# Kernel optimization log

Measured on AMD Instinct MI355X. Metric: run time of the kernel, lower is better.

## Reference

```python
import jax, jax.numpy as jnp
import numpy as np

B, T, D = 2, 2048, 2048
NH, NKV = 16, 4
HD = D // NH  # 128
BASE, TSL = 10000.0, 1024


def rotary_tables(T, hd, base=BASE, tsl=TSL):
    # Matches Rotary.forward with rd == hd (rd=0 in __init__ -> full head dim).
    ar = jnp.arange(0, hd, 2, dtype=jnp.float32) / hd
    if T <= tsl:
        inv = 1.0 / (base ** ar)
    else:
        # NTK-style rescale; note right-assoc exponent in original torch code:
        # 1/(base * (T/tsl) ** ((rd/(rd-2)) ** ar))
        inv = 1.0 / (base * jnp.power(T / tsl, jnp.power(hd / (hd - 2.0), ar)))
    f = jnp.outer(jnp.arange(T, dtype=jnp.float32), inv)  # [T, hd//2]
    cos = jnp.cos(f)[None, :, None, :]  # [1,T,1,hd//2]
    sin = jnp.sin(f)[None, :, None, :]
    return cos, sin


def apply_rope(x, cos, sin):
    # full-dim rope: split halves, rotate
    h = x.shape[-1] // 2
    x1, x2 = x[..., :h], x[..., h:]
    return jnp.concatenate((x1 * cos + x2 * sin, -x1 * sin + x2 * cos), axis=-1)


def rms_norm(x):
    eps = jnp.finfo(x.dtype).eps
    return x * jax.lax.rsqrt(jnp.mean(x * x, axis=-1, keepdims=True) + eps)


def setup_inputs() -> dict:
    key = jax.random.key(0)
    k0, k1, k2, k3, k4 = jax.random.split(key, 5)
    s = 0.02
    return {
        "x": jax.random.normal(k0, (B, T, D), jnp.float32),
        "qw": jax.random.normal(k1, (NH * HD, D), jnp.float32) * s,
        "kw": jax.random.normal(k2, (NKV * HD, D), jnp.float32) * s,
        "vw": jax.random.normal(k3, (NKV * HD, D), jnp.float32) * s,
        "ow": jax.random.normal(k4, (D, D), jnp.float32) * s,
        "qg": jnp.ones((NH,), jnp.float32),
    }


def reference(x, qw, kw, vw, ow, qg):
    Bx, Tx, Dx = x.shape
    q = (x @ qw.T).reshape(Bx, Tx, NH, HD)
    k = (x @ kw.T).reshape(Bx, Tx, NKV, HD)
    v = (x @ vw.T).reshape(Bx, Tx, NKV, HD)
    q = rms_norm(q)
    k = rms_norm(k)
    cos, sin = rotary_tables(Tx, HD)
    q = apply_rope(q, cos, sin) * qg[None, None, :, None]
    k = apply_rope(k, cos, sin)
    # GQA: repeat kv heads
    r = NH // NKV
    k = jnp.repeat(k, r, axis=2)  # [B,T,NH,HD]
    v = jnp.repeat(v, r, axis=2)
    scale = 1.0 / jnp.sqrt(jnp.asarray(HD, q.dtype))
    scores = jnp.einsum("bqhd,bkhd->bhqk", q, k) * scale  # [B,NH,T,T]
    causal = jnp.tril(jnp.ones((Tx, Tx), dtype=bool))
    scores = jnp.where(causal[None, None, :, :], scores, jnp.asarray(-jnp.inf, scores.dtype))
    attn = jax.nn.softmax(scores, axis=-1)
    y = jnp.einsum("bhqk,bkhd->bqhd", attn, v)  # [B,T,NH,HD]
    return y.reshape(Bx, Tx, Dx) @ ow.T
```

## Files before the change

### kernel.cpp

```cpp
#include <hip/hip_runtime.h>
#include <hip/hip_bf16.h>
#include <stdint.h>


typedef __attribute__((ext_vector_type(8))) short short8;
typedef __attribute__((ext_vector_type(4))) float f32x4;
typedef __attribute__((ext_vector_type(16))) float f32x16;

#define GLOAD16(gp, lp) \
  __builtin_amdgcn_global_load_lds((const __attribute__((address_space(1))) void*)(gp), \
                                   (__attribute__((address_space(3))) void*)(lp), 16, 0, 0)

#define BAR() do { asm volatile("" ::: "memory"); __builtin_amdgcn_s_barrier(); asm volatile("" ::: "memory"); } while (0)

__device__ __forceinline__ float bf2f(unsigned short u) {
  union { unsigned int i; float f; } v; v.i = ((unsigned int)u) << 16; return v.f;
}
__device__ __forceinline__ unsigned short f2bf(float f) {
  union { float fl; unsigned int i; } v; v.fl = f;
  unsigned int r = v.i + 0x7fffu + ((v.i >> 16) & 1u);
  return (unsigned short)(r >> 16);
}
__device__ __forceinline__ unsigned pk2(float a, float b) {
  return (unsigned)f2bf(a) | ((unsigned)f2bf(b) << 16);
}

__global__ __launch_bounds__(256) void prep_kernel(
    const float* __restrict__ x, const float* __restrict__ qw,
    const float* __restrict__ kw, const float* __restrict__ vw,
    const float* __restrict__ ow,
    unsigned short* __restrict__ xb, unsigned short* __restrict__ wqkv,
    unsigned short* __restrict__ owb, float* __restrict__ cost, float* __restrict__ sint) {
  const int NX = 2097152;
  const int NW = 1572864;
  const int NO = 1048576;
  const int NT = 131072;
  int tid = blockIdx.x * 256 + threadIdx.x;
  if (tid < NX) {
    float4 v = ((const float4*)x)[tid];
    uint2 o; o.x = pk2(v.x, v.y); o.y = pk2(v.z, v.w);
    ((uint2*)xb)[tid] = o;
  } else if (tid < NX + NW) {
    int i = tid - NX; int e = i * 4;
    const float* src = (e < 4194304) ? (qw + e)
                     : (e < 5242880) ? (kw + (e - 4194304))
                                     : (vw + (e - 5242880));
    float4 v = *(const float4*)src;
    uint2 o; o.x = pk2(v.x, v.y); o.y = pk2(v.z, v.w);
    ((uint2*)wqkv)[i] = o;
  } else if (tid < NX + NW + NO) {
    int i = tid - NX - NW;
    float4 v = ((const float4*)ow)[i];
    uint2 o; o.x = pk2(v.x, v.y); o.y = pk2(v.z, v.w);
    ((uint2*)owb)[i] = o;
  } else if (tid < NX + NW + NO + NT) {
    int i = tid - NX - NW - NO;
    int t = i >> 6, j = i & 63;
    float e = exp2f(0.02272008f * (float)j * (1.0f / 64.0f));
    float inv = 1.0f / (10000.0f * exp2f(e));
    float f = (float)t * inv;
    cost[i] = cosf(f);
    sint[i] = sinf(f);
  }
}

template <int IM, int OUTF>
__global__ __launch_bounds__(512) void gemm8ph(const unsigned short* __restrict__ A,
                                               const unsigned short* __restrict__ Bw,
                                               void* __restrict__ Cp,
                                               int MT, int NTn, int N, int K) {
  extern __shared__ char smc[];
  constexpr int S = IM * 8;
  constexpr int IQ = IM / 2;
  constexpr int ASZ = IM * 2048;
  constexpr int DB = 2 * ASZ + 32768;
  constexpr int AL = (IM * 128) / 512;
  const int tid = threadIdx.x;
  const int l = tid & 63, w = tid >> 6;
  const int lane_r = l & 15, lane_g = l >> 4;
  const int wr = w >> 2, wc = w & 3;

  int qch = (MT * NTn) >> 3;
  int orig = blockIdx.x;
  int wgid = (orig & 7) * qch + (orig >> 3);
  int by = wgid / NTn, bx = wgid - by * NTn;
  const int m0 = by * IM * 32, n0 = bx * 256;

  f32x4 acc[IM][4];
#pragma unroll
  for (int i = 0; i < IM; ++i)
#pragma unroll
    for (int j = 0; j < 4; ++j) acc[i][j] = {0.f, 0.f, 0.f, 0.f};

  const unsigned short* srcA[AL]; int ldA[AL];
#pragma unroll
  for (int t = 0; t < AL; ++t) {
    int idx = t * 512 + tid;
    int rc = idx >> 3, kc = idx & 7;
    int wrp = rc >= S ? 1 : 0, rr = rc & (S - 1);
    int row = wrp * 2 * S + rr;
    srcA[t] = A + (size_t)(m0 + row) * K + (kc ^ (rc & 7)) * 8;
    ldA[t] = idx * 16;
  }
  const unsigned short* srcB[2]; int ldB[2];
#pragma unroll
  for (int t = 0; t < 2; ++t) {
    int idx = t * 512 + tid;
    int rc = idx >> 3, kc = idx & 7;
    int nrow = (rc >> 5) * 64 + (rc & 31);
    srcB[t] = Bw + (size_t)(n0 + nrow) * K + (kc ^ (rc & 7)) * 8;
    ldB[t] = idx * 16;
  }
  const int SK = S * K, JK = 32 * K;

  auto STA = [&](int kt, int ih, int dqb) {
    char* d = smc + dqb + ih * ASZ;
#pragma unroll
    for (int t = 0; t < AL; ++t) GLOAD16(srcA[t] + kt + ih * SK, d + ldA[t]);
  };
  auto STB = [&](int kt, int jh, int dqb) {
    char* d = smc + dqb + 2 * ASZ + jh * 16384;
#pragma unroll
    for (int t = 0; t < 2; ++t) GLOAD16(srcB[t] + kt + jh * JK, d + ldB[t]);
  };

  int oA[IQ][2], oB[2][2];
#pragma unroll
  for (int iq = 0; iq < IQ; ++iq)
#pragma unroll
    for (int ks = 0; ks < 2; ++ks) {
      int rc = wr * S + iq * 16 + lane_r;
      oA[iq][ks] = rc * 128 + ((ks * 64 + lane_g * 16) ^ ((rc & 7) << 4));
    }
#pragma unroll
  for (int jj = 0; jj < 2; ++jj)
#pragma unroll
    for (int ks = 0; ks < 2; ++ks) {
      int rc = wc * 32 + jj * 16 + lane_r;
      oB[jj][ks] = rc * 128 + ((ks * 64 + lane_g * 16) ^ ((rc & 7) << 4));
    }

#define VMC() do { if constexpr (IM == 8) asm volatile("s_waitcnt vmcnt(6)" ::: "memory"); \
                   else                   asm volatile("s_waitcnt vmcnt(5)" ::: "memory"); } while (0)
#define VM0() asm volatile("s_waitcnt vmcnt(0)" ::: "memory")
#define MM(IH, JH, BR) do { \
    __builtin_amdgcn_s_setprio(1); \
    _Pragma("unroll") \
    for (int iq = 0; iq < IQ; ++iq) \
      _Pragma("unroll") \
      for (int jj = 0; jj < 2; ++jj) \
        _Pragma("unroll") \
        for (int ks = 0; ks < 2; ++ks) \
          acc[(IH) * IQ + iq][(JH) * 2 + jj] = __builtin_amdgcn_mfma_f32_16x16x32_bf16( \
              af[iq][ks], BR[jj][ks], acc[(IH) * IQ + iq][(JH) * 2 + jj], 0, 0, 0); \
    __builtin_amdgcn_s_setprio(0); } while (0)

  const int NS = K >> 6;
  STA(0, 0, 0); STB(0, 0, 0); STB(0, 1, 0); STA(0, 1, 0);
  STA(64, 0, DB); STB(64, 0, DB); STB(64, 1, DB);
  VMC();
  BAR();

#pragma unroll 1
  for (int s = 0; s < NS; ++s) {
    const int dq = (s & 1) * DB, dn = DB - dq;
    const char* Ab = smc + dq;
    const char* Bb = Ab + 2 * ASZ;
    short8 af[IQ][2], b0[2][2], b1[2][2];
    if (s + 1 < NS) STA((s + 1) << 6, 1, dn);
#pragma unroll
    for (int iq = 0; iq < IQ; ++iq)
#pragma unroll
      for (int ks = 0; ks < 2; ++ks) af[iq][ks] = *(const short8*)(Ab + oA[iq][ks]);
#pragma unroll
    for (int jj = 0; jj < 2; ++jj)
#pragma unroll
      for (int ks = 0; ks < 2; ++ks) b0[jj][ks] = *(const short8*)(Bb + oB[jj][ks]);
    MM(0, 0, b0);
    BAR();
    if (s + 2 < NS) STA((s + 2) << 6, 0, dq);
#pragma unroll
    for (int jj = 0; jj < 2; ++jj)
#pragma unroll
      for (int ks = 0; ks < 2; ++ks) b1[jj][ks] = *(const short8*)(Bb + 16384 + oB[jj][ks]);
    MM(0, 1, b1);
    BAR();
    if (s + 2 < NS) STB((s + 2) << 6, 0, dq);
#pragma unroll
    for (int iq = 0; iq < IQ; ++iq)
#pragma unroll
      for (int ks = 0; ks < 2; ++ks) af[iq][ks] = *(const short8*)(Ab + ASZ + oA[iq][ks]);
    MM(1, 0, b0);
    BAR();
    if (s + 2 < NS) STB((s + 2) << 6, 1, dq);
    MM(1, 1, b1);
    if (s + 2 < NS) VMC(); else VM0();
    BAR();
  }
#undef VMC
#undef VM0
#undef MM

#pragma unroll
  for (int ih = 0; ih < 2; ++ih)
#pragma unroll
    for (int iq = 0; iq < IQ; ++iq) {
      int row = m0 + wr * 2 * S + ih * S + iq * 16 + lane_g * 4;
#pragma unroll
      for (int j = 0; j < 4; ++j) {
        int col = n0 + wc * 64 + j * 16 + lane_r;
#pragma unroll
        for (int r = 0; r < 4; ++r) {
          float v = acc[ih * IQ + iq][j][r];
          if (OUTF)
            ((float*)Cp)[(size_t)(row + r) * N + col] = v;
          else
            ((unsigned short*)Cp)[(size_t)(row + r) * N + col] = f2bf(v);
        }
      }
    }
}

__global__ __launch_bounds__(256) void normrope_kernel(unsigned short* __restrict__ qkv,
                                                       const float* __restrict__ cost,
                                                       const float* __restrict__ sint,
                                                       const float* __restrict__ qg) {
  const int tid = threadIdx.x, l = tid & 63, w = tid >> 6;
  int row = blockIdx.x * 4 + w;
  int tok = row / 20, hh = row - tok * 20;
  int t = tok & 2047;
  bool isq = hh < 16;
  int col0 = isq ? hh * 128 : 2048 + (hh - 16) * 128;
  unsigned short* p = qkv + (size_t)tok * 3072 + col0 + 2 * l;
  unsigned int u = *(const unsigned int*)p;
  float x0 = bf2f((unsigned short)(u & 0xffffu));
  float x1 = bf2f((unsigned short)(u >> 16));
  float ss = x0 * x0 + x1 * x1;
#pragma unroll
  for (int m = 1; m < 64; m <<= 1) ss += __shfl_xor(ss, m);
  float rn = rsqrtf(ss * (1.0f / 128.0f) + 1.1920928955078125e-07f);
  float n0 = x0 * rn, n1 = x1 * rn;
  float p0 = __shfl_xor(n0, 32);
  float p1 = __shfl_xor(n1, 32);
  int jj = (2 * l) & 63;
  float c0 = cost[t * 64 + jj], c1 = cost[t * 64 + jj + 1];
  float s0 = sint[t * 64 + jj], s1 = sint[t * 64 + jj + 1];
  float o0, o1;
  if (l < 32) { o0 = n0 * c0 + p0 * s0; o1 = n1 * c1 + p1 * s1; }
  else        { o0 = -p0 * s0 + n0 * c0; o1 = -p1 * s1 + n1 * c1; }
  if (isq) { float g = qg[hh] * 0.08838834764831845f * 1.4426950408889634f; o0 *= g; o1 *= g; }
  *(unsigned int*)p = pk2(o0, o1);
}

__global__ __launch_bounds__(256) void vtrans_kernel(const unsigned short* __restrict__ qkv,
                                                     unsigned short* __restrict__ vtg) {
  __shared__ unsigned short tile[64][132];
  int bid = blockIdx.x;
  int pan = bid & 7, tt = bid >> 3;
  int b = pan >> 2, kvh = pan & 3;
  int t0 = tt * 64;
  const unsigned short* src = qkv + ((size_t)(b * 2048 + t0)) * 3072 + 2560 + kvh * 128;
#pragma unroll
  for (int i = 0; i < 8; ++i) {
    int idx = i * 256 + threadIdx.x;
    int row = idx >> 5, c4 = idx & 31;
    uint2 v = *(const uint2*)(src + (size_t)row * 3072 + c4 * 4);
    *(uint2*)&tile[row][c4 * 4] = v;
  }
  __syncthreads();
  unsigned short* dst = vtg + (size_t)pan * 262144 + t0;
#pragma unroll
  for (int i = 0; i < 8; ++i) {
    int idx = i * 256 + threadIdx.x;
    int d = idx >> 4, tc = idx & 15;
    unsigned short a0 = tile[tc * 4 + 0][d], a1 = tile[tc * 4 + 1][d];
    unsigned short a2 = tile[tc * 4 + 2][d], a3 = tile[tc * 4 + 3][d];
    uint2 o; o.x = (unsigned)a0 | ((unsigned)a1 << 16);
    o.y = (unsigned)a2 | ((unsigned)a3 << 16);
    *(uint2*)(dst + (size_t)d * 2048 + tc * 4) = o;
  }
}

__global__ __launch_bounds__(256, 2) void attn_fa5(const unsigned short* __restrict__ qkv,
                                                   const unsigned short* __restrict__ vtg,
                                                   unsigned short* __restrict__ y) {
  extern __shared__ char smc[];
  const int tid = threadIdx.x;
  const int l = tid & 63, w = tid >> 6;
  const int lq = l & 31, hi = l >> 5;

  int n = blockIdx.x;
  int pan = n & 7;
  int b = pan >> 2, kvh = pan & 3;
  int idx2 = n >> 3;
  int h = kvh * 4 + (idx2 & 3);
  int pairIdx = idx2 >> 2;
  const size_t rowbase = (size_t)b * 2048;
  const unsigned short* kvK = qkv + rowbase * 3072;
  const unsigned short* vtp = vtg + (size_t)pan * 262144;

  int kg[4], vg[4], sl[4];
#pragma unroll
  for (int t = 0; t < 4; ++t) {
    int idx = t * 256 + tid;
    { int row = idx >> 4, c = idx & 15, gc = c ^ (row & 7);
      kg[t] = row * 3072 + 2048 + kvh * 128 + gc * 8; }
    { int d = idx >> 3, c = idx & 7, gc = c ^ (d & 7);
      vg[t] = d * 2048 + gc * 8; }
    sl[t] = idx * 16;
  }
  const int swq = (lq & 7) << 4;
  int oxd[8];
#pragma unroll
  for (int ds = 0; ds < 8; ++ds) oxd[ds] = (ds * 32 + hi * 16) ^ swq;
  const int krow = lq * 256;
  const int vrow = lq * 128;
  const int pbase = 65536 + w * 4096;
  const int prow = pbase + lq * 128;
  int opw[2][4];
#pragma unroll
  for (int t = 0; t < 2; ++t)
#pragma unroll
    for (int m = 0; m < 4; ++m) opw[t][m] = prow + ((t * 64 + m * 16 + hi * 8) ^ swq);

  auto STAGE = [&](int tile, int bufsel) {
    const unsigned short* srcK = kvK + (size_t)tile * 64 * 3072;
    const unsigned short* srcV = vtp + tile * 64;
    char* kd = smc + bufsel * 16384;
    char* vd = smc + 32768 + bufsel * 16384;
#pragma unroll
    for (int t = 0; t < 4; ++t) {
      GLOAD16(srcK + kg[t], kd + sl[t]);
      GLOAD16(srcV + vg[t], vd + sl[t]);
    }
  };

#pragma unroll 1
  for (int phase = 0; phase < 2; ++phase) {
    const int qt = phase ? pairIdx : 15 - pairIdx;
    const int q0 = qt * 128;
    const int nkb = 2 * qt + 2;
    const int wrow0 = q0 + w * 32;
    const int qrow = wrow0 + lq;

    STAGE(0, 0);
    short8 qf[8];
#pragma unroll
    for (int ds = 0; ds < 8; ++ds)
      qf[ds] = *(const short8*)(qkv + (rowbase + qrow) * 3072 + h * 128 + ds * 16 + hi * 8);

    f32x16 acc[4];
#pragma unroll
    for (int dt = 0; dt < 4; ++dt)
#pragma unroll
      for (int jj = 0; jj < 16; ++jj) acc[dt][jj] = 0.f;
    float mrun = -1e30f, lrun = 0.f;

    __syncthreads();

#pragma unroll 1
    for (int kb = 0; kb < nkb; ++kb) {
      const int cur = kb & 1;
      if (kb + 1 < nkb) STAGE(kb + 1, cur ^ 1);
      const int j0 = kb * 64;
      if (j0 <= wrow0 + 31) {
        const int kbb = cur * 16384;
        const int vbb = 32768 + cur * 16384;
        f32x16 s0, s1;
#pragma unroll
        for (int jj = 0; jj < 16; ++jj) { s0[jj] = 0.f; s1[jj] = 0.f; }
        __builtin_amdgcn_s_setprio(1);
#pragma unroll
        for (int ds = 0; ds < 8; ++ds) {
          short8 kf = *(const short8*)(smc + kbb + krow + oxd[ds]);
          s0 = __builtin_amdgcn_mfma_f32_32x32x16_bf16(kf, qf[ds], s0, 0, 0, 0);
        }
#pragma unroll
        for (int ds = 0; ds < 8; ++ds) {
          short8 kf = *(const short8*)(smc + kbb + 8192 + krow + oxd[ds]);
          s1 = __builtin_amdgcn_mfma_f32_32x32x16_bf16(kf, qf[ds], s1, 0, 0, 0);
        }
        __builtin_amdgcn_s_setprio(0);
        const int rq = qrow - j0;
        if (j0 + 63 > wrow0) {
#pragma unroll
          for (int jj = 0; jj < 16; ++jj) {
            int kl = (jj & 3) + 8 * (jj >> 2) + 4 * hi;
            s0[jj] = (kl > rq) ? -1e30f : s0[jj];
            s1[jj] = (kl + 32 > rq) ? -1e30f : s1[jj];
          }
        }
        float pmax = s0[0];
#pragma unroll
        for (int jj = 0; jj < 16; ++jj) pmax = fmaxf(pmax, fmaxf(s0[jj], s1[jj]));
        pmax = fmaxf(pmax, __shfl_xor(pmax, 32));
        if (!__all(pmax - mrun <= 11.5f)) {
          float mn = fmaxf(mrun, pmax);
          float corr = exp2f(mrun - mn);
          lrun *= corr;
#pragma unroll
          for (int dt = 0; dt < 4; ++dt)
#pragma unroll
            for (int jj = 0; jj < 16; ++jj) acc[dt][jj] *= corr;
          mrun = mn;
        }
        float rs = 0.f;
#pragma unroll
        for (int jj = 0; jj < 16; ++jj) {
          s0[jj] = exp2f(s0[jj] - mrun); rs += s0[jj];
          s1[jj] = exp2f(s1[jj] - mrun); rs += s1[jj];
        }
        rs += __shfl_xor(rs, 32);
        lrun += rs;
#pragma unroll
        for (int m = 0; m < 4; ++m) {
          uint2 p0, p1;
          p0.x = pk2(s0[4 * m], s0[4 * m + 1]); p0.y = pk2(s0[4 * m + 2], s0[4 * m + 3]);
          p1.x = pk2(s1[4 * m], s1[4 * m + 1]); p1.y = pk2(s1[4 * m + 2], s1[4 * m + 3]);
          *(uint2*)(smc + opw[0][m]) = p0;
          *(uint2*)(smc + opw[1][m]) = p1;
        }
        short8 pfr[4];
#pragma unroll
        for (int ksl = 0; ksl < 4; ++ksl)
          pfr[ksl] = *(const short8*)(smc + prow + oxd[ksl]);
        __builtin_amdgcn_s_setprio(1);
#pragma unroll
        for (int ksl = 0; ksl < 4; ++ksl)
#pragma unroll
          for (int dt = 0; dt < 4; ++dt) {
            short8 vf = *(const short8*)(smc + vbb + dt * 4096 + vrow + oxd[ksl]);
            acc[dt] = __builtin_amdgcn_mfma_f32_32x32x16_bf16(vf, pfr[ksl], acc[dt], 0, 0, 0);
          }
        __builtin_amdgcn_s_setprio(0);
      }
      __syncthreads();
    }
    float linv = 1.0f / lrun;
    unsigned short* yrow = y + (rowbase + qrow) * 2048 + h * 128;
#pragma unroll
    for (int dt = 0; dt < 4; ++dt)
#pragma unroll
      for (int m = 0; m < 4; ++m) {
        uint2 o;
        o.x = pk2(acc[dt][4 * m] * linv, acc[dt][4 * m + 1] * linv);
        o.y = pk2(acc[dt][4 * m + 2] * linv, acc[dt][4 * m + 3] * linv);
        *(uint2*)(yrow + dt * 32 + m * 8 + hi * 4) = o;
      }
  }
}

extern "C" void kernel_launch(void* const* d_in, const int* in_sizes, int n_in,
                              void* d_out, int out_size, void* d_ws, size_t ws_size,
                              hipStream_t stream) {
  (void)in_sizes; (void)n_in; (void)out_size; (void)ws_size;
  const float* x  = (const float*)d_in[0];
  const float* qw = (const float*)d_in[1];
  const float* kw = (const float*)d_in[2];
  const float* vw = (const float*)d_in[3];
  const float* ow = (const float*)d_in[4];
  const float* qg = (const float*)d_in[5];

  char* ws = (char*)d_ws;
  unsigned short* xb   = (unsigned short*)(ws + 0);
  unsigned short* vtg  = (unsigned short*)(ws + 0);
  unsigned short* wqkv = (unsigned short*)(ws + 16777216);
  unsigned short* owb  = (unsigned short*)(ws + 29360128);
  unsigned short* qkvb = (unsigned short*)(ws + 37748736);
  unsigned short* y    = (unsigned short*)(ws + 62914560);
  float* cost          = (float*)(ws + 79691776);
  float* sint          = (float*)(ws + 80216064);

  prep_kernel<<<18944, 256, 0, stream>>>(x, qw, kw, vw, ow, xb, wqkv, owb, cost, sint);
  gemm8ph<8, 0><<<192, 512, 131072, stream>>>(xb, wqkv, qkvb, 16, 12, 3072, 2048);
  normrope_kernel<<<20480, 256, 0, stream>>>(qkvb, cost, sint, qg);
  vtrans_kernel<<<256, 256, 0, stream>>>(qkvb, vtg);
  attn_fa5<<<256, 256, 81920, stream>>>(qkvb, vtg, y);
  gemm8ph<4, 1><<<256, 512, 98304, stream>>>(y, owb, d_out, 32, 8, 2048, 2048);
}
```

Baseline: 214.6 us.

## Retile QKV GEMM, fuse norm-rope with V transpose, split attention phases

The GEMM is generalized with a template N-tile width. The QKV projection now runs as 256 blocks of 128x384 instead of 192 blocks of 256x256, which fills more compute units. The norm/rope and V-transpose kernels are merged into one launch, which is safe because the transpose only reads V columns that norm/rope never touches. Attention now launches one block per causal q-tile instead of looping over two phases per block, giving 512 blocks. It also builds the P operand in registers with bf16 packing and permlane32 swaps rather than staging it through LDS, which frees 16KB of shared memory per block. The risks are a lane-layout mistake in the permlane-built P fragments and load imbalance across causal tiles now that each block handles only one of them.

Measured after the change: 196.1 us. 1.09x faster.

```diff
diff --git a/kernel.cpp b/kernel.cpp
--- a/kernel.cpp
+++ b/kernel.cpp
@@ -64,7 +64,7 @@
   }
 }
 
-template <int IM, int OUTF>
+template <int IM, int NB, int OUTF>
 __global__ __launch_bounds__(512) void gemm8ph(const unsigned short* __restrict__ A,
                                                const unsigned short* __restrict__ Bw,
                                                void* __restrict__ Cp,
@@ -72,9 +72,13 @@
   extern __shared__ char smc[];
   constexpr int S = IM * 8;
   constexpr int IQ = IM / 2;
+  constexpr int JQ = NB / 128;
   constexpr int ASZ = IM * 2048;
-  constexpr int DB = 2 * ASZ + 32768;
+  constexpr int BSZ = NB * 64;
+  constexpr int DB = 2 * ASZ + 2 * BSZ;
   constexpr int AL = (IM * 128) / 512;
+  constexpr int BL = NB / 128;
+  constexpr int VMCN = AL + 2 * BL;
   const int tid = threadIdx.x;
   const int l = tid & 63, w = tid >> 6;
   const int lane_r = l & 15, lane_g = l >> 4;
@@ -84,13 +88,13 @@
   int orig = blockIdx.x;
   int wgid = (orig & 7) * qch + (orig >> 3);
   int by = wgid / NTn, bx = wgid - by * NTn;
-  const int m0 = by * IM * 32, n0 = bx * 256;
-
-  f32x4 acc[IM][4];
+  const int m0 = by * IM * 32, n0 = bx * NB;
+
+  f32x4 acc[IM][2 * JQ];
 #pragma unroll
   for (int i = 0; i < IM; ++i)
 #pragma unroll
-    for (int j = 0; j < 4; ++j) acc[i][j] = {0.f, 0.f, 0.f, 0.f};
+    for (int j = 0; j < 2 * JQ; ++j) acc[i][j] = {0.f, 0.f, 0.f, 0.f};
 
   const unsigned short* srcA[AL]; int ldA[AL];
 #pragma unroll
@@ -102,16 +106,17 @@
     srcA[t] = A + (size_t)(m0 + row) * K + (kc ^ (rc & 7)) * 8;
     ldA[t] = idx * 16;
   }
-  const unsigned short* srcB[2]; int ldB[2];
-#pragma unroll
-  for (int t = 0; t < 2; ++t) {
+  const unsigned short* srcB[BL]; int ldB[BL];
+#pragma unroll
+  for (int t = 0; t < BL; ++t) {
     int idx = t * 512 + tid;
     int rc = idx >> 3, kc = idx & 7;
-    int nrow = (rc >> 5) * 64 + (rc & 31);
+    int g16 = rc >> 4;
+    int nrow = (g16 / JQ) * (NB / 4) + (g16 % JQ) * 16 + (rc & 15);
     srcB[t] = Bw + (size_t)(n0 + nrow) * K + (kc ^ (rc & 7)) * 8;
     ldB[t] = idx * 16;
   }
-  const int SK = S * K, JK = 32 * K;
+  const int SK = S * K, JK = (NB / 8) * K;
 
   auto STA = [&](int kt, int ih, int dqb) {
     char* d = smc + dqb + ih * ASZ;
@@ -119,12 +124,12 @@
     for (int t = 0; t < AL; ++t) GLOAD16(srcA[t] + kt + ih * SK, d + ldA[t]);
   };
   auto STB = [&](int kt, int jh, int dqb) {
-    char* d = smc + dqb + 2 * ASZ + jh * 16384;
-#pragma unroll
-    for (int t = 0; t < 2; ++t) GLOAD16(srcB[t] + kt + jh * JK, d + ldB[t]);
+    char* d = smc + dqb + 2 * ASZ + jh * BSZ;
+#pragma unroll
+    for (int t = 0; t < BL; ++t) GLOAD16(srcB[t] + kt + jh * JK, d + ldB[t]);
   };
 
-  int oA[IQ][2], oB[2][2];
+  int oA[IQ][2], oB[JQ][2];
 #pragma unroll
   for (int iq = 0; iq < IQ; ++iq)
 #pragma unroll
@@ -133,26 +138,25 @@
       oA[iq][ks] = rc * 128 + ((ks * 64 + lane_g * 16) ^ ((rc & 7) << 4));
     }
 #pragma unroll
-  for (int jj = 0; jj < 2; ++jj)
+  for (int jj = 0; jj < JQ; ++jj)
 #pragma unroll
     for (int ks = 0; ks < 2; ++ks) {
-      int rc = wc * 32 + jj * 16 + lane_r;
+      int rc = wc * (NB / 8) + jj * 16 + lane_r;
       oB[jj][ks] = rc * 128 + ((ks * 64 + lane_g * 16) ^ ((rc & 7) << 4));
     }
 
-#define VMC() do { if constexpr (IM == 8) asm volatile("s_waitcnt vmcnt(6)" ::: "memory"); \
-                   else                   asm volatile("s_waitcnt vmcnt(5)" ::: "memory"); } while (0)
+#define VMC() asm volatile("s_waitcnt vmcnt(%0)" :: "i"(VMCN) : "memory")
 #define VM0() asm volatile("s_waitcnt vmcnt(0)" ::: "memory")
 #define MM(IH, JH, BR) do { \
     __builtin_amdgcn_s_setprio(1); \
     _Pragma("unroll") \
     for (int iq = 0; iq < IQ; ++iq) \
       _Pragma("unroll") \
-      for (int jj = 0; jj < 2; ++jj) \
+      for (int jj = 0; jj < JQ; ++jj) \
         _Pragma("unroll") \
         for (int ks = 0; ks < 2; ++ks) \
-          acc[(IH) * IQ + iq][(JH) * 2 + jj] = __builtin_amdgcn_mfma_f32_16x16x32_bf16( \
-              af[iq][ks], BR[jj][ks], acc[(IH) * IQ + iq][(JH) * 2 + jj], 0, 0, 0); \
+          acc[(IH) * IQ + iq][(JH) * JQ + jj] = __builtin_amdgcn_mfma_f32_16x16x32_bf16( \
+              af[iq][ks], BR[jj][ks], acc[(IH) * IQ + iq][(JH) * JQ + jj], 0, 0, 0); \
     __builtin_amdgcn_s_setprio(0); } while (0)
 
   const int NS = K >> 6;
@@ -166,23 +170,23 @@
     const int dq = (s & 1) * DB, dn = DB - dq;
     const char* Ab = smc + dq;
     const char* Bb = Ab + 2 * ASZ;
-    short8 af[IQ][2], b0[2][2], b1[2][2];
+    short8 af[IQ][2], b0[JQ][2], b1[JQ][2];
     if (s + 1 < NS) STA((s + 1) << 6, 1, dn);
 #pragma unroll
     for (int iq = 0; iq < IQ; ++iq)
 #pragma unroll
       for (int ks = 0; ks < 2; ++ks) af[iq][ks] = *(const short8*)(Ab + oA[iq][ks]);
 #pragma unroll
-    for (int jj = 0; jj < 2; ++jj)
+    for (int jj = 0; jj < JQ; ++jj)
 #pragma unroll
       for (int ks = 0; ks < 2; ++ks) b0[jj][ks] = *(const short8*)(Bb + oB[jj][ks]);
     MM(0, 0, b0);
     BAR();
     if (s + 2 < NS) STA((s + 2) << 6, 0, dq);
 #pragma unroll
-    for (int jj = 0; jj < 2; ++jj)
-#pragma unroll
-      for (int ks = 0; ks < 2; ++ks) b1[jj][ks] = *(const short8*)(Bb + 16384 + oB[jj][ks]);
+    for (int jj = 0; jj < JQ; ++jj)
+#pragma unroll
+      for (int ks = 0; ks < 2; ++ks) b1[jj][ks] = *(const short8*)(Bb + BSZ + oB[jj][ks]);
     MM(0, 1, b1);
     BAR();
     if (s + 2 < NS) STB((s + 2) << 6, 0, dq);
@@ -207,81 +211,85 @@
     for (int iq = 0; iq < IQ; ++iq) {
       int row = m0 + wr * 2 * S + ih * S + iq * 16 + lane_g * 4;
 #pragma unroll
-      for (int j = 0; j < 4; ++j) {
-        int col = n0 + wc * 64 + j * 16 + lane_r;
-#pragma unroll
-        for (int r = 0; r < 4; ++r) {
-          float v = acc[ih * IQ + iq][j][r];
-          if (OUTF)
-            ((float*)Cp)[(size_t)(row + r) * N + col] = v;
-          else
-            ((unsigned short*)Cp)[(size_t)(row + r) * N + col] = f2bf(v);
+      for (int jh = 0; jh < 2; ++jh)
+#pragma unroll
+        for (int jj = 0; jj < JQ; ++jj) {
+          int col = n0 + wc * (NB / 4) + jh * (NB / 8) + jj * 16 + lane_r;
+#pragma unroll
+          for (int r = 0; r < 4; ++r) {
+            float v = acc[ih * IQ + iq][jh * JQ + jj][r];
+            if (OUTF)
+              ((float*)Cp)[(size_t)(row + r) * N + col] = v;
+            else
+              ((unsigned short*)Cp)[(size_t)(row + r) * N + col] = f2bf(v);
+          }
         }
-      }
-    }
-}
-
-__global__ __launch_bounds__(256) void normrope_kernel(unsigned short* __restrict__ qkv,
-                                                       const float* __restrict__ cost,
-                                                       const float* __restrict__ sint,
-                                                       const float* __restrict__ qg) {
-  const int tid = threadIdx.x, l = tid & 63, w = tid >> 6;
-  int row = blockIdx.x * 4 + w;
-  int tok = row / 20, hh = row - tok * 20;
-  int t = tok & 2047;
-  bool isq = hh < 16;
-  int col0 = isq ? hh * 128 : 2048 + (hh - 16) * 128;
-  unsigned short* p = qkv + (size_t)tok * 3072 + col0 + 2 * l;
-  unsigned int u = *(const unsigned int*)p;
-  float x0 = bf2f((unsigned short)(u & 0xffffu));
-  float x1 = bf2f((unsigned short)(u >> 16));
-  float ss = x0 * x0 + x1 * x1;
-#pragma unroll
-  for (int m = 1; m < 64; m <<= 1) ss += __shfl_xor(ss, m);
-  float rn = rsqrtf(ss * (1.0f / 128.0f) + 1.1920928955078125e-07f);
-  float n0 = x0 * rn, n1 = x1 * rn;
-  float p0 = __shfl_xor(n0, 32);
-  float p1 = __shfl_xor(n1, 32);
-  int jj = (2 * l) & 63;
-  float c0 = cost[t * 64 + jj], c1 = cost[t * 64 + jj + 1];
-  float s0 = sint[t * 64 + jj], s1 = sint[t * 64 + jj + 1];
-  float o0, o1;
-  if (l < 32) { o0 = n0 * c0 + p0 * s0; o1 = n1 * c1 + p1 * s1; }
-  else        { o0 = -p0 * s0 + n0 * c0; o1 = -p1 * s1 + n1 * c1; }
-  if (isq) { float g = qg[hh] * 0.08838834764831845f * 1.4426950408889634f; o0 *= g; o1 *= g; }
-  *(unsigned int*)p = pk2(o0, o1);
-}
-
-__global__ __launch_bounds__(256) void vtrans_kernel(const unsigned short* __restrict__ qkv,
-                                                     unsigned short* __restrict__ vtg) {
+    }
+}
+
+__global__ __launch_bounds__(256) void normrope_vt_kernel(unsigned short* __restrict__ qkv,
+                                                          const float* __restrict__ cost,
+                                                          const float* __restrict__ sint,
+                                                          const float* __restrict__ qg,
+                                                          unsigned short* __restrict__ vtg) {
   __shared__ unsigned short tile[64][132];
   int bid = blockIdx.x;
-  int pan = bid & 7, tt = bid >> 3;
-  int b = pan >> 2, kvh = pan & 3;
-  int t0 = tt * 64;
-  const unsigned short* src = qkv + ((size_t)(b * 2048 + t0)) * 3072 + 2560 + kvh * 128;
-#pragma unroll
-  for (int i = 0; i < 8; ++i) {
-    int idx = i * 256 + threadIdx.x;
-    int row = idx >> 5, c4 = idx & 31;
-    uint2 v = *(const uint2*)(src + (size_t)row * 3072 + c4 * 4);
-    *(uint2*)&tile[row][c4 * 4] = v;
-  }
-  __syncthreads();
-  unsigned short* dst = vtg + (size_t)pan * 262144 + t0;
-#pragma unroll
-  for (int i = 0; i < 8; ++i) {
-    int idx = i * 256 + threadIdx.x;
-    int d = idx >> 4, tc = idx & 15;
-    unsigned short a0 = tile[tc * 4 + 0][d], a1 = tile[tc * 4 + 1][d];
-    unsigned short a2 = tile[tc * 4 + 2][d], a3 = tile[tc * 4 + 3][d];
-    uint2 o; o.x = (unsigned)a0 | ((unsigned)a1 << 16);
-    o.y = (unsigned)a2 | ((unsigned)a3 << 16);
-    *(uint2*)(dst + (size_t)d * 2048 + tc * 4) = o;
-  }
-}
-
-__global__ __launch_bounds__(256, 2) void attn_fa5(const unsigned short* __restrict__ qkv,
+  const int tid = threadIdx.x;
+  if (bid < 20480) {
+    const int l = tid & 63, w = tid >> 6;
+    int row = bid * 4 + w;
+    int tok = row / 20, hh = row - tok * 20;
+    int t = tok & 2047;
+    bool isq = hh < 16;
+    int col0 = isq ? hh * 128 : 2048 + (hh - 16) * 128;
+    unsigned short* p = qkv + (size_t)tok * 3072 + col0 + 2 * l;
+    unsigned int u = *(const unsigned int*)p;
+    float x0 = bf2f((unsigned short)(u & 0xffffu));
+    float x1 = bf2f((unsigned short)(u >> 16));
+    float ss = x0 * x0 + x1 * x1;
+#pragma unroll
+    for (int m = 1; m < 64; m <<= 1) ss += __shfl_xor(ss, m);
+    float rn = rsqrtf(ss * (1.0f / 128.0f) + 1.1920928955078125e-07f);
+    float n0 = x0 * rn, n1 = x1 * rn;
+    float p0 = __shfl_xor(n0, 32);
+    float p1 = __shfl_xor(n1, 32);
+    int jj = (2 * l) & 63;
+    float c0 = cost[t * 64 + jj], c1 = cost[t * 64 + jj + 1];
+    float s0 = sint[t * 64 + jj], s1 = sint[t * 64 + jj + 1];
+    float o0, o1;
+    if (l < 32) { o0 = n0 * c0 + p0 * s0; o1 = n1 * c1 + p1 * s1; }
+    else        { o0 = -p0 * s0 + n0 * c0; o1 = -p1 * s1 + n1 * c1; }
+    if (isq) { float g = qg[hh] * 0.08838834764831845f * 1.4426950408889634f; o0 *= g; o1 *= g; }
+    *(unsigned int*)p = pk2(o0, o1);
+  } else {
+    int bid2 = bid - 20480;
+    int pan = bid2 & 7, tt = bid2 >> 3;
+    int b = pan >> 2, kvh = pan & 3;
+    int t0 = tt * 64;
+    const unsigned short* src = qkv + ((size_t)(b * 2048 + t0)) * 3072 + 2560 + kvh * 128;
+#pragma unroll
+    for (int i = 0; i < 8; ++i) {
+      int idx = i * 256 + tid;
+      int row = idx >> 5, c4 = idx & 31;
+      uint2 v = *(const uint2*)(src + (size_t)row * 3072 + c4 * 4);
+      *(uint2*)&tile[row][c4 * 4] = v;
+    }
+    __syncthreads();
+    unsigned short* dst = vtg + (size_t)pan * 262144 + t0;
+#pragma unroll
+    for (int i = 0; i < 8; ++i) {
+      int idx = i * 256 + tid;
+      int d = idx >> 4, tc = idx & 15;
+      unsigned short a0 = tile[tc * 4 + 0][d], a1 = tile[tc * 4 + 1][d];
+      unsigned short a2 = tile[tc * 4 + 2][d], a3 = tile[tc * 4 + 3][d];
+      uint2 o; o.x = (unsigned)a0 | ((unsigned)a1 << 16);
+      o.y = (unsigned)a2 | ((unsigned)a3 << 16);
+      *(uint2*)(dst + (size_t)d * 2048 + tc * 4) = o;
+    }
+  }
+}
+
+__global__ __launch_bounds__(256, 2) void attn_fa8(const unsigned short* __restrict__ qkv,
                                                    const unsigned short* __restrict__ vtg,
                                                    unsigned short* __restrict__ y) {
   extern __shared__ char smc[];
@@ -289,12 +297,14 @@
   const int l = tid & 63, w = tid >> 6;
   const int lq = l & 31, hi = l >> 5;
 
-  int n = blockIdx.x;
-  int pan = n & 7;
+  int bid = blockIdx.x;
+  int n8 = bid & 255;
+  int pan = n8 & 7;
   int b = pan >> 2, kvh = pan & 3;
-  int idx2 = n >> 3;
+  int idx2 = n8 >> 3;
   int h = kvh * 4 + (idx2 & 3);
   int pairIdx = idx2 >> 2;
+  const int qt = (bid >> 8) ? pairIdx : 15 - pairIdx;
   const size_t rowbase = (size_t)b * 2048;
   const unsigned short* kvK = qkv + rowbase * 3072;
   const unsigned short* vtp = vtg + (size_t)pan * 262144;
@@ -315,13 +325,6 @@
   for (int ds = 0; ds < 8; ++ds) oxd[ds] = (ds * 32 + hi * 16) ^ swq;
   const int krow = lq * 256;
   const int vrow = lq * 128;
-  const int pbase = 65536 + w * 4096;
-  const int prow = pbase + lq * 128;
-  int opw[2][4];
-#pragma unroll
-  for (int t = 0; t < 2; ++t)
-#pragma unroll
-    for (int m = 0; m < 4; ++m) opw[t][m] = prow + ((t * 64 + m * 16 + hi * 8) ^ swq);
 
   auto STAGE = [&](int tile, int bufsel) {
     const unsigned short* srcK = kvK + (size_t)tile * 64 * 3072;
@@ -335,119 +338,121 @@
     }
   };
 
+  const int q0 = qt * 128;
+  const int nkb = 2 * qt + 2;
+  const int wrow0 = q0 + w * 32;
+  const int qrow = wrow0 + lq;
+
+  STAGE(0, 0);
+  short8 qf[8];
+#pragma unroll
+  for (int ds = 0; ds < 8; ++ds)
+    qf[ds] = *(const short8*)(qkv + (rowbase + qrow) * 3072 + h * 128 + ds * 16 + hi * 8);
+
+  f32x16 acc[4];
+#pragma unroll
+  for (int dt = 0; dt < 4; ++dt)
+#pragma unroll
+    for (int jj = 0; jj < 16; ++jj) acc[dt][jj] = 0.f;
+  float mrun = -1e30f, lrun = 0.f;
+
+  __syncthreads();
+
 #pragma unroll 1
-  for (int phase = 0; phase < 2; ++phase) {
-    const int qt = phase ? pairIdx : 15 - pairIdx;
-    const int q0 = qt * 128;
-    const int nkb = 2 * qt + 2;
-    const int wrow0 = q0 + w * 32;
-    const int qrow = wrow0 + lq;
-
-    STAGE(0, 0);
-    short8 qf[8];
-#pragma unroll
-    for (int ds = 0; ds < 8; ++ds)
-      qf[ds] = *(const short8*)(qkv + (rowbase + qrow) * 3072 + h * 128 + ds * 16 + hi * 8);
-
-    f32x16 acc[4];
-#pragma unroll
-    for (int dt = 0; dt < 4; ++dt)
-#pragma unroll
-      for (int jj = 0; jj < 16; ++jj) acc[dt][jj] = 0.f;
-    float mrun = -1e30f, lrun = 0.f;
-
+  for (int kb = 0; kb < nkb; ++kb) {
+    const int cur = kb & 1;
+    if (kb + 1 < nkb) STAGE(kb + 1, cur ^ 1);
+    const int j0 = kb * 64;
+    if (j0 <= wrow0 + 31) {
+      const int kbb = cur * 16384;
+      const int vbb = 32768 + cur * 16384;
+      f32x16 s0, s1;
+#pragma unroll
+      for (int jj = 0; jj < 16; ++jj) { s0[jj] = 0.f; s1[jj] = 0.f; }
+      __builtin_amdgcn_s_setprio(1);
+#pragma unroll
+      for (int ds = 0; ds < 8; ++ds) {
+        short8 kf = *(const short8*)(smc + kbb + krow + oxd[ds]);
+        s0 = __builtin_amdgcn_mfma_f32_32x32x16_bf16(kf, qf[ds], s0, 0, 0, 0);
+      }
+#pragma unroll
+      for (int ds = 0; ds < 8; ++ds) {
+        short8 kf = *(const short8*)(smc + kbb + 8192 + krow + oxd[ds]);
+        s1 = __builtin_amdgcn_mfma_f32_32x32x16_bf16(kf, qf[ds], s1, 0, 0, 0);
+      }
+      __builtin_amdgcn_s_setprio(0);
+      const int rq = qrow - j0;
+      if (j0 + 63 > wrow0) {
+#pragma unroll
+        for (int jj = 0; jj < 16; ++jj) {
+          int kl = (jj & 3) + 8 * (jj >> 2) + 4 * hi;
+          s0[jj] = (kl > rq) ? -1e30f : s0[jj];
+          s1[jj] = (kl + 32 > rq) ? -1e30f : s1[jj];
+        }
+      }
+      float pmax = s0[0];
+#pragma unroll
+      for (int jj = 0; jj < 16; ++jj) pmax = fmaxf(pmax, fmaxf(s0[jj], s1[jj]));
+      pmax = fmaxf(pmax, __shfl_xor(pmax, 32));
+      if (!__all(pmax - mrun <= 11.5f)) {
+        float mn = fmaxf(mrun, pmax);
+        float corr = exp2f(mrun - mn);
+        lrun *= corr;
+#pragma unroll
+        for (int dt = 0; dt < 4; ++dt)
+#pragma unroll
+          for (int jj = 0; jj < 16; ++jj) acc[dt][jj] *= corr;
+        mrun = mn;
+      }
+      float rs = 0.f;
+#pragma unroll
+      for (int jj = 0; jj < 16; ++jj) {
+        s0[jj] = exp2f(s0[jj] - mrun); rs += s0[jj];
+        s1[jj] = exp2f(s1[jj] - mrun); rs += s1[jj];
+      }
+      rs += __shfl_xor(rs, 32);
+      lrun += rs;
+      unsigned r0[8], r1[8];
+#pragma unroll
+      for (int j = 0; j < 4; ++j) {
+        asm("v_cvt_pk_bf16_f32 %0, %1, %2" : "=v"(r0[2 * j]) : "v"(s0[4 * j]), "v"(s0[4 * j + 1]));
+        asm("v_cvt_pk_bf16_f32 %0, %1, %2" : "=v"(r0[2 * j + 1]) : "v"(s0[4 * j + 2]), "v"(s0[4 * j + 3]));
+        asm("v_cvt_pk_bf16_f32 %0, %1, %2" : "=v"(r1[2 * j]) : "v"(s1[4 * j]), "v"(s1[4 * j + 1]));
+        asm("v_cvt_pk_bf16_f32 %0, %1, %2" : "=v"(r1[2 * j + 1]) : "v"(s1[4 * j + 2]), "v"(s1[4 * j + 3]));
+      }
+      __builtin_amdgcn_s_setprio(1);
+#pragma unroll
+      for (int ksl = 0; ksl < 4; ++ksl) {
+        unsigned* rr = (ksl < 2) ? r0 : r1;
+        int kk = ksl & 1;
+        unsigned w0 = rr[4 * kk], w2 = rr[4 * kk + 2];
+        asm("v_permlane32_swap_b32 %0, %1" : "+v"(w0), "+v"(w2));
+        unsigned w1 = rr[4 * kk + 1], w3 = rr[4 * kk + 3];
+        asm("v_permlane32_swap_b32 %0, %1" : "+v"(w1), "+v"(w3));
+        union { unsigned u[4]; short8 s8; } pu;
+        pu.u[0] = w0; pu.u[1] = w1; pu.u[2] = w2; pu.u[3] = w3;
+        short8 pf = pu.s8;
+#pragma unroll
+        for (int dt = 0; dt < 4; ++dt) {
+          short8 vf = *(const short8*)(smc + vbb + dt * 4096 + vrow + oxd[ksl]);
+          acc[dt] = __builtin_amdgcn_mfma_f32_32x32x16_bf16(vf, pf, acc[dt], 0, 0, 0);
+        }
+      }
+      __builtin_amdgcn_s_setprio(0);
+    }
     __syncthreads();
-
-#pragma unroll 1
-    for (int kb = 0; kb < nkb; ++kb) {
-      const int cur = kb & 1;
-      if (kb + 1 < nkb) STAGE(kb + 1, cur ^ 1);
-      const int j0 = kb * 64;
-      if (j0 <= wrow0 + 31) {
-        const int kbb = cur * 16384;
-        const int vbb = 32768 + cur * 16384;
-        f32x16 s0, s1;
-#pragma unroll
-        for (int jj = 0; jj < 16; ++jj) { s0[jj] = 0.f; s1[jj] = 0.f; }
-        __builtin_amdgcn_s_setprio(1);
-#pragma unroll
-        for (int ds = 0; ds < 8; ++ds) {
-          short8 kf = *(const short8*)(smc + kbb + krow + oxd[ds]);
-          s0 = __builtin_amdgcn_mfma_f32_32x32x16_bf16(kf, qf[ds], s0, 0, 0, 0);
-        }
-#pragma unroll
-        for (int ds = 0; ds < 8; ++ds) {
-          short8 kf = *(const short8*)(smc + kbb + 8192 + krow + oxd[ds]);
-          s1 = __builtin_amdgcn_mfma_f32_32x32x16_bf16(kf, qf[ds], s1, 0, 0, 0);
-        }
-        __builtin_amdgcn_s_setprio(0);
-        const int rq = qrow - j0;
-        if (j0 + 63 > wrow0) {
-#pragma unroll
-          for (int jj = 0; jj < 16; ++jj) {
-            int kl = (jj & 3) + 8 * (jj >> 2) + 4 * hi;
-            s0[jj] = (kl > rq) ? -1e30f : s0[jj];
-            s1[jj] = (kl + 32 > rq) ? -1e30f : s1[jj];
-          }
-        }
-        float pmax = s0[0];
-#pragma unroll
-        for (int jj = 0; jj < 16; ++jj) pmax = fmaxf(pmax, fmaxf(s0[jj], s1[jj]));
-        pmax = fmaxf(pmax, __shfl_xor(pmax, 32));
-        if (!__all(pmax - mrun <= 11.5f)) {
-          float mn = fmaxf(mrun, pmax);
-          float corr = exp2f(mrun - mn);
-          lrun *= corr;
-#pragma unroll
-          for (int dt = 0; dt < 4; ++dt)
-#pragma unroll
-            for (int jj = 0; jj < 16; ++jj) acc[dt][jj] *= corr;
-          mrun = mn;
-        }
-        float rs = 0.f;
-#pragma unroll
-        for (int jj = 0; jj < 16; ++jj) {
-          s0[jj] = exp2f(s0[jj] - mrun); rs += s0[jj];
-          s1[jj] = exp2f(s1[jj] - mrun); rs += s1[jj];
-        }
-        rs += __shfl_xor(rs, 32);
-        lrun += rs;
-#pragma unroll
-        for (int m = 0; m < 4; ++m) {
-          uint2 p0, p1;
-          p0.x = pk2(s0[4 * m], s0[4 * m + 1]); p0.y = pk2(s0[4 * m + 2], s0[4 * m + 3]);
-          p1.x = pk2(s1[4 * m], s1[4 * m + 1]); p1.y = pk2(s1[4 * m + 2], s1[4 * m + 3]);
-          *(uint2*)(smc + opw[0][m]) = p0;
-          *(uint2*)(smc + opw[1][m]) = p1;
-        }
-        short8 pfr[4];
-#pragma unroll
-        for (int ksl = 0; ksl < 4; ++ksl)
-          pfr[ksl] = *(const short8*)(smc + prow + oxd[ksl]);
-        __builtin_amdgcn_s_setprio(1);
-#pragma unroll
-        for (int ksl = 0; ksl < 4; ++ksl)
-#pragma unroll
-          for (int dt = 0; dt < 4; ++dt) {
-            short8 vf = *(const short8*)(smc + vbb + dt * 4096 + vrow + oxd[ksl]);
-            acc[dt] = __builtin_amdgcn_mfma_f32_32x32x16_bf16(vf, pfr[ksl], acc[dt], 0, 0, 0);
-          }
-        __builtin_amdgcn_s_setprio(0);
-      }
-      __syncthreads();
-    }
-    float linv = 1.0f / lrun;
-    unsigned short* yrow = y + (rowbase + qrow) * 2048 + h * 128;
-#pragma unroll
-    for (int dt = 0; dt < 4; ++dt)
-#pragma unroll
-      for (int m = 0; m < 4; ++m) {
-        uint2 o;
-        o.x = pk2(acc[dt][4 * m] * linv, acc[dt][4 * m + 1] * linv);
-        o.y = pk2(acc[dt][4 * m + 2] * linv, acc[dt][4 * m + 3] * linv);
-        *(uint2*)(yrow + dt * 32 + m * 8 + hi * 4) = o;
-      }
-  }
+  }
+  float linv = 1.0f / lrun;
+  unsigned short* yrow = y + (rowbase + qrow) * 2048 + h * 128;
+#pragma unroll
+  for (int dt = 0; dt < 4; ++dt)
+#pragma unroll
+    for (int m = 0; m < 4; ++m) {
+      uint2 o;
+      o.x = pk2(acc[dt][4 * m] * linv, acc[dt][4 * m + 1] * linv);
+      o.y = pk2(acc[dt][4 * m + 2] * linv, acc[dt][4 * m + 3] * linv);
+      *(uint2*)(yrow + dt * 32 + m * 8 + hi * 4) = o;
+    }
 }
 
 extern "C" void kernel_launch(void* const* d_in, const int* in_sizes, int n_in,
@@ -472,9 +477,8 @@
   float* sint          = (float*)(ws + 80216064);
 
   prep_kernel<<<18944, 256, 0, stream>>>(x, qw, kw, vw, ow, xb, wqkv, owb, cost, sint);
-  gemm8ph<8, 0><<<192, 512, 131072, stream>>>(xb, wqkv, qkvb, 16, 12, 3072, 2048);
-  normrope_kernel<<<20480, 256, 0, stream>>>(qkvb, cost, sint, qg);
-  vtrans_kernel<<<256, 256, 0, stream>>>(qkvb, vtg);
-  attn_fa5<<<256, 256, 81920, stream>>>(qkvb, vtg, y);
-  gemm8ph<4, 1><<<256, 512, 98304, stream>>>(y, owb, d_out, 32, 8, 2048, 2048);
-}
+  gemm8ph<4, 384, 0><<<256, 512, 131072, stream>>>(xb, wqkv, qkvb, 32, 8, 3072, 2048);
+  normrope_vt_kernel<<<20736, 256, 0, stream>>>(qkvb, cost, sint, qg, vtg);
+  attn_fa8<<<512, 256, 65536, stream>>>(qkvb, vtg, y);
+  gemm8ph<4, 256, 1><<<256, 512, 98304, stream>>>(y, owb, d_out, 32, 8, 2048, 2048);
+}
```
